# Performance work log

Hardware: AMD Instinct MI355X
Metric: run time of the kernel (lower is better)

The kernel has to match this reference:

```python
import jax, jax.numpy as jnp
import numpy as np

K = 10        # n_functions (random MLP draws)
H = 20        # hidden width of each tiny per-feature MLP
LN_EPS = 1e-5 # torch LayerNorm default eps
STD_EPS = 1e-8


def _layernorm(h):
    # LayerNorm over last dim, affine weight=1, bias=0 (torch default init),
    # biased variance, eps=1e-5.
    mu = h.mean(-1, keepdims=True)
    var = ((h - mu) ** 2).mean(-1, keepdims=True)
    return (h - mu) * jax.lax.rsqrt(var + LN_EPS)


def setup_inputs() -> dict:
    key = jax.random.key(0)
    B, T, N = 128, 256, 16
    ks = jax.random.split(key, 7)
    inputs = jax.random.normal(ks[0], (B, T, N), dtype=jnp.float32)

    def u(k, shape, bound):
        return jax.random.uniform(k, shape, minval=-bound, maxval=bound, dtype=jnp.float32)

    # torch Linear default init: uniform(-1/sqrt(fan_in), 1/sqrt(fan_in)) for W and b
    W1 = u(ks[1], (K, N, H), 1.0)        # Linear(1,20): fan_in=1
    b1 = u(ks[2], (K, N, H), 1.0)
    bnd = 1.0 / np.sqrt(H)
    W2 = u(ks[3], (K, N, H, H), bnd)     # Linear(20,20), weight layout [out,in]
    b2 = u(ks[4], (K, N, H), bnd)
    W3 = u(ks[5], (K, N, H), bnd)        # Linear(20,1) weight squeezed to [H]
    b3 = u(ks[6], (K, N), bnd)
    return {"inputs": inputs, "W1": W1, "b1": b1, "W2": W2, "b2": b2, "W3": W3, "b3": b3}


def reference(inputs, W1, b1, W2, b2, W3, b3):
    x = inputs.astype(jnp.float32)
    # standardize over batch dim (torch .std is unbiased, ddof=1)
    x = (x - x.mean(0)) / x.std(0, ddof=1)

    # All K draws x all N per-feature MLPs as one batched computation.
    # h: [K, B, T, N, H]
    h = jax.nn.relu(x[None, ..., None] * W1[:, None, None] + b1[:, None, None])
    h = _layernorm(h)
    h = jax.nn.relu(jnp.einsum('kbtni,knoi->kbtno', h, W2) + b2[:, None, None])
    h = _layernorm(h)
    t = jnp.einsum('kbtni,kni->kbtn', h, W3) + b3[:, None, None]   # [K, B, T, N]

    # std_out: standardize over batch dim
    t = (t - t.mean(1, keepdims=True)) / (t.std(1, ddof=1, keepdims=True) + STD_EPS)

    m_marginals = t.mean(1)                   # [K, T, N]
    prod_marginals = jnp.prod(m_marginals, -1)  # [K, T]
    prod_joint = jnp.prod(t, -1).mean(1)        # [K, T]
    per_k_mse = jnp.mean((prod_marginals - prod_joint) ** 2, axis=-1)  # [K]
    return jnp.mean(per_k_mse)
```

## Files before the change

kernel.cpp:

```cpp
#include <hip/hip_runtime.h>
#include <math.h>

#define B_ 128
#define T_ 256
#define N_ 16
#define K_ 10
#define H_ 20
#define TN_ 4096
#define TQ_ 128

#define REP20(F) F(0) F(1) F(2) F(3) F(4) F(5) F(6) F(7) F(8) F(9) \
                 F(10) F(11) F(12) F(13) F(14) F(15) F(16) F(17) F(18) F(19)

__device__ __forceinline__ float wsum(float v)
{
#pragma unroll
    for (int off = 32; off; off >>= 1) v += __shfl_xor(v, off);
    return v;
}

__global__ __launch_bounds__(256, 3) void k_all(
    const float* __restrict__ x,
    const float* __restrict__ W1, const float* __restrict__ b1,
    const float* __restrict__ W2, const float* __restrict__ b2,
    const float* __restrict__ W3, const float* __restrict__ b3,
    float* __restrict__ out)
{
    __shared__ float xz[32 * 129];
    __shared__ float zl[32 * 128];
    __shared__ float pjp[4];

    const int tq  = blockIdx.x;
    const int k   = blockIdx.y;
    const int tid = threadIdx.x;
    const int wv  = tid >> 6;
    const int l   = tid & 63;

#pragma unroll
    for (int r = 0; r < 4; ++r) {
        const int g4 = r * 1024 + tid * 4;
        const int b  = g4 >> 5;
        const int d0 = g4 & 31;
        const float4 v = *reinterpret_cast<const float4*>(x + b * TN_ + tq * 32 + d0);
        xz[(d0 + 0) * 129 + b] = v.x;
        xz[(d0 + 1) * 129 + b] = v.y;
        xz[(d0 + 2) * 129 + b] = v.z;
        xz[(d0 + 3) * 129 + b] = v.w;
    }
    __syncthreads();

#pragma unroll
    for (int c = 0; c < 8; ++c) {
        const int col = wv * 8 + c;
        const float a0 = xz[col * 129 + l];
        const float a1 = xz[col * 129 + 64 + l];
        const float mu = wsum(a0 + a1) * (1.f / 128.f);
        const float d0 = a0 - mu, d1 = a1 - mu;
        const float r  = __builtin_amdgcn_rsqf(wsum(fmaf(d0, d0, d1 * d1)) * (1.f / 127.f));
        xz[col * 129 + l]      = d0 * r;
        xz[col * 129 + 64 + l] = d1 * r;
    }
    __syncthreads();

#pragma unroll 1
    for (int it = 0; it < 8; ++it) {
        const int col = wv * 8 + it;
        const int kn  = k * 16 + (col & 15);

        const float u0 = xz[col * 129 + l];
        const float u1 = xz[col * 129 + 64 + l];

        const float4* __restrict__ w1v = reinterpret_cast<const float4*>(W1 + kn * 20);
        const float4* __restrict__ b1v = reinterpret_cast<const float4*>(b1 + kn * 20);
        const float4* __restrict__ w2v = reinterpret_cast<const float4*>(W2 + kn * 400);
        const float4* __restrict__ b2v = reinterpret_cast<const float4*>(b2 + kn * 20);
        const float4* __restrict__ w3v = reinterpret_cast<const float4*>(W3 + kn * 20);
        const float  bb3 = b3[kn];

#define DECLH(i) float ha##i, hb##i;
        REP20(DECLH)
        float s1a = 0.f, s1b = 0.f;
#define L1C(c,i0,i1,i2,i3) { const float4 w = w1v[c]; const float4 bb = b1v[c]; \
        ha##i0 = fmaxf(fmaf(u0, w.x, bb.x), 0.f); hb##i0 = fmaxf(fmaf(u1, w.x, bb.x), 0.f); s1a += ha##i0; s1b += hb##i0; \
        ha##i1 = fmaxf(fmaf(u0, w.y, bb.y), 0.f); hb##i1 = fmaxf(fmaf(u1, w.y, bb.y), 0.f); s1a += ha##i1; s1b += hb##i1; \
        ha##i2 = fmaxf(fmaf(u0, w.z, bb.z), 0.f); hb##i2 = fmaxf(fmaf(u1, w.z, bb.z), 0.f); s1a += ha##i2; s1b += hb##i2; \
        ha##i3 = fmaxf(fmaf(u0, w.w, bb.w), 0.f); hb##i3 = fmaxf(fmaf(u1, w.w, bb.w), 0.f); s1a += ha##i3; s1b += hb##i3; }
        L1C(0,0,1,2,3) L1C(1,4,5,6,7) L1C(2,8,9,10,11) L1C(3,12,13,14,15) L1C(4,16,17,18,19)

        const float mu1a = s1a * 0.05f, mu1b = s1b * 0.05f;
        float v1a = 0.f, v1b = 0.f;
#define VAR1(i) { float d = ha##i - mu1a; v1a = fmaf(d, d, v1a); d = hb##i - mu1b; v1b = fmaf(d, d, v1b); }
        REP20(VAR1)
        const float r1a = __builtin_amdgcn_rsqf(v1a * 0.05f + 1e-5f);
        const float r1b = __builtin_amdgcn_rsqf(v1b * 0.05f + 1e-5f);
        const float m1a = mu1a * r1a, m1b = mu1b * r1b;
#define NRM1(i) ha##i = fmaf(ha##i, r1a, -m1a); hb##i = fmaf(hb##i, r1b, -m1b);
        REP20(NRM1)

#define DECLG(i) float ga##i, gb##i;
        REP20(DECLG)
        float s2a = 0.f, s2b = 0.f;
#define L2C(o,c,i0,i1,i2,i3) { const float4 w = w2v[(o) * 5 + (c)]; \
        acca = fmaf(ha##i0, w.x, acca); acca = fmaf(ha##i1, w.y, acca); \
        acca = fmaf(ha##i2, w.z, acca); acca = fmaf(ha##i3, w.w, acca); \
        accb = fmaf(hb##i0, w.x, accb); accb = fmaf(hb##i1, w.y, accb); \
        accb = fmaf(hb##i2, w.z, accb); accb = fmaf(hb##i3, w.w, accb); }
#define L2ROW(o,bo) { float acca = (bo), accb = (bo); \
        L2C(o,0,0,1,2,3) L2C(o,1,4,5,6,7) L2C(o,2,8,9,10,11) \
        L2C(o,3,12,13,14,15) L2C(o,4,16,17,18,19) \
        ga##o = fmaxf(acca, 0.f); s2a += ga##o; gb##o = fmaxf(accb, 0.f); s2b += gb##o; }
        {
            const float4 b2c0 = b2v[0], b2c1 = b2v[1], b2c2 = b2v[2], b2c3 = b2v[3], b2c4 = b2v[4];
            L2ROW(0,  b2c0.x) L2ROW(1,  b2c0.y) L2ROW(2,  b2c0.z) L2ROW(3,  b2c0.w)
            L2ROW(4,  b2c1.x) L2ROW(5,  b2c1.y) L2ROW(6,  b2c1.z) L2ROW(7,  b2c1.w)
            L2ROW(8,  b2c2.x) L2ROW(9,  b2c2.y) L2ROW(10, b2c2.z) L2ROW(11, b2c2.w)
            L2ROW(12, b2c3.x) L2ROW(13, b2c3.y) L2ROW(14, b2c3.z) L2ROW(15, b2c3.w)
            L2ROW(16, b2c4.x) L2ROW(17, b2c4.y) L2ROW(18, b2c4.z) L2ROW(19, b2c4.w)
        }

        const float mu2a = s2a * 0.05f, mu2b = s2b * 0.05f;
        float v2a = 0.f, v2b = 0.f;
#define VAR2(i) { float d = ga##i - mu2a; v2a = fmaf(d, d, v2a); d = gb##i - mu2b; v2b = fmaf(d, d, v2b); }
        REP20(VAR2)
        const float r2a = __builtin_amdgcn_rsqf(v2a * 0.05f + 1e-5f);
        const float r2b = __builtin_amdgcn_rsqf(v2b * 0.05f + 1e-5f);
        const float m2a = mu2a * r2a, m2b = mu2b * r2b;

        float t0 = bb3, t1 = bb3;
#define L3C(c,i0,i1,i2,i3) { const float4 w = w3v[c]; \
        t0 = fmaf(fmaf(ga##i0, r2a, -m2a), w.x, t0); t1 = fmaf(fmaf(gb##i0, r2b, -m2b), w.x, t1); \
        t0 = fmaf(fmaf(ga##i1, r2a, -m2a), w.y, t0); t1 = fmaf(fmaf(gb##i1, r2b, -m2b), w.y, t1); \
        t0 = fmaf(fmaf(ga##i2, r2a, -m2a), w.z, t0); t1 = fmaf(fmaf(gb##i2, r2b, -m2b), w.z, t1); \
        t0 = fmaf(fmaf(ga##i3, r2a, -m2a), w.w, t0); t1 = fmaf(fmaf(gb##i3, r2b, -m2b), w.w, t1); }
        L3C(0,0,1,2,3) L3C(1,4,5,6,7) L3C(2,8,9,10,11) L3C(3,12,13,14,15) L3C(4,16,17,18,19)

        const float smu = wsum(t0 + t1) * (1.f / 128.f);
        const float e0 = t0 - smu, e1 = t1 - smu;
        const float sd = sqrtf(wsum(fmaf(e0, e0, e1 * e1)) * (1.f / 127.f));
        const float rr = 1.f / (sd + 1e-8f);
        zl[col * 128 + l]      = e0 * rr;
        zl[col * 128 + 64 + l] = e1 * rr;
    }
    __syncthreads();

    {
        const int t_loc = wv >> 1;
        const int b     = (wv & 1) * 64 + l;
        float pj = zl[(t_loc * 16 + 0) * 128 + b];
#pragma unroll
        for (int n = 1; n < 16; ++n) pj *= zl[(t_loc * 16 + n) * 128 + b];
        const float ps = wsum(pj);
        if (l == 0) pjp[wv] = ps;
    }
    __syncthreads();
    if (tid < 2) {
        const float pjm = (pjp[tid * 2] + pjp[tid * 2 + 1]) * (1.f / 128.f);
        atomicAdd(out, pjm * pjm * (1.f / (K_ * T_)));
    }
}

extern "C" void kernel_launch(void* const* d_in, const int* in_sizes, int n_in,
                              void* d_out, int out_size, void* d_ws, size_t ws_size,
                              hipStream_t stream)
{
    const float* x  = (const float*)d_in[0];
    const float* W1 = (const float*)d_in[1];
    const float* b1 = (const float*)d_in[2];
    const float* W2 = (const float*)d_in[3];
    const float* b2 = (const float*)d_in[4];
    const float* W3 = (const float*)d_in[5];
    const float* b3 = (const float*)d_in[6];
    float* out = (float*)d_out;

    hipMemsetAsync(out, 0, sizeof(float), stream);

    dim3 grid(TQ_, K_);
    k_all<<<grid, 256, 0, stream>>>(x, W1, b1, W2, b2, W3, b3, out);
}
```

Measured before the change: 236.4 us.

## Split blocks by (k,n) feature with global z buffer and last-block ticket reduction

Reorganizes the grid so each block handles one (k,n) MLP over a 32-timestep slab, which keeps that MLP's weights uniform per block and lets them be scalar-loaded instead of varying per wavefront. Standardized outputs go to a global workspace buffer. A ticket counter picks the last of 16 feature blocks for each slab to compute the product-over-N reduction, and a done counter finalizes the output. The cost is global-memory round trips for z, strided scalar input gathers, atomic and fence synchronization, a grid of only 1280 blocks, and launch bounds lowered to a single block per SIMD.

```diff
diff --git a/kernel.cpp b/kernel.cpp
--- a/kernel.cpp
+++ b/kernel.cpp
@@ -7,7 +7,8 @@
 #define K_ 10
 #define H_ 20
 #define TN_ 4096
-#define TQ_ 128
+#define TSLAB_ 32
+#define NTC_ 8
 
 #define REP20(F) F(0) F(1) F(2) F(3) F(4) F(5) F(6) F(7) F(8) F(9) \
                  F(10) F(11) F(12) F(13) F(14) F(15) F(16) F(17) F(18) F(19)
@@ -19,73 +20,64 @@
     return v;
 }
 
-__global__ __launch_bounds__(256, 3) void k_all(
+__global__ __launch_bounds__(256, 1) void k_fused(
     const float* __restrict__ x,
     const float* __restrict__ W1, const float* __restrict__ b1,
     const float* __restrict__ W2, const float* __restrict__ b2,
     const float* __restrict__ W3, const float* __restrict__ b3,
-    float* __restrict__ out)
+    float* __restrict__ out,
+    unsigned int* __restrict__ tickets,
+    unsigned int* __restrict__ done,
+    float* __restrict__ acc,
+    float* __restrict__ zbuf)
 {
-    __shared__ float xz[32 * 129];
-    __shared__ float zl[32 * 128];
-    __shared__ float pjp[4];
+    __shared__ float xz[TSLAB_ * 129];
+    __shared__ float wred[4];
+    __shared__ int   flag;
 
-    const int tq  = blockIdx.x;
-    const int k   = blockIdx.y;
+    const int tc  = blockIdx.x;
+    const int kn  = blockIdx.y;
+    const int k   = kn >> 4;
+    const int n   = kn & 15;
     const int tid = threadIdx.x;
     const int wv  = tid >> 6;
     const int l   = tid & 63;
 
 #pragma unroll
-    for (int r = 0; r < 4; ++r) {
-        const int g4 = r * 1024 + tid * 4;
-        const int b  = g4 >> 5;
-        const int d0 = g4 & 31;
-        const float4 v = *reinterpret_cast<const float4*>(x + b * TN_ + tq * 32 + d0);
-        xz[(d0 + 0) * 129 + b] = v.x;
-        xz[(d0 + 1) * 129 + b] = v.y;
-        xz[(d0 + 2) * 129 + b] = v.z;
-        xz[(d0 + 3) * 129 + b] = v.w;
+    for (int it = 0; it < 16; ++it) {
+        const int e   = it * 256 + tid;
+        const int col = e >> 7;
+        const int b   = e & 127;
+        xz[col * 129 + b] = x[b * TN_ + (tc * TSLAB_ + col) * N_ + n];
     }
     __syncthreads();
 
-#pragma unroll
-    for (int c = 0; c < 8; ++c) {
-        const int col = wv * 8 + c;
-        const float a0 = xz[col * 129 + l];
-        const float a1 = xz[col * 129 + 64 + l];
-        const float mu = wsum(a0 + a1) * (1.f / 128.f);
-        const float d0 = a0 - mu, d1 = a1 - mu;
-        const float r  = __builtin_amdgcn_rsqf(wsum(fmaf(d0, d0, d1 * d1)) * (1.f / 127.f));
-        xz[col * 129 + l]      = d0 * r;
-        xz[col * 129 + 64 + l] = d1 * r;
-    }
-    __syncthreads();
+    const float* __restrict__ w1c = W1 + kn * H_;
+    const float* __restrict__ b1c = b1 + kn * H_;
+    const float* __restrict__ w2c = W2 + kn * H_ * H_;
+    const float* __restrict__ b2c = b2 + kn * H_;
+    const float* __restrict__ w3c = W3 + kn * H_;
+    const float  bb3 = b3[kn];
 
 #pragma unroll 1
     for (int it = 0; it < 8; ++it) {
         const int col = wv * 8 + it;
-        const int kn  = k * 16 + (col & 15);
+        const int tg  = tc * TSLAB_ + col;
 
-        const float u0 = xz[col * 129 + l];
-        const float u1 = xz[col * 129 + 64 + l];
-
-        const float4* __restrict__ w1v = reinterpret_cast<const float4*>(W1 + kn * 20);
-        const float4* __restrict__ b1v = reinterpret_cast<const float4*>(b1 + kn * 20);
-        const float4* __restrict__ w2v = reinterpret_cast<const float4*>(W2 + kn * 400);
-        const float4* __restrict__ b2v = reinterpret_cast<const float4*>(b2 + kn * 20);
-        const float4* __restrict__ w3v = reinterpret_cast<const float4*>(W3 + kn * 20);
-        const float  bb3 = b3[kn];
+        const float a0 = xz[col * 129 + l];
+        const float a1 = xz[col * 129 + 64 + l];
+        const float xmu = wsum(a0 + a1) * (1.f / 128.f);
+        const float xd0 = a0 - xmu, xd1 = a1 - xmu;
+        const float xr  = __builtin_amdgcn_rsqf(wsum(fmaf(xd0, xd0, xd1 * xd1)) * (1.f / 127.f));
+        const float u0 = xd0 * xr, u1 = xd1 * xr;
 
 #define DECLH(i) float ha##i, hb##i;
         REP20(DECLH)
         float s1a = 0.f, s1b = 0.f;
-#define L1C(c,i0,i1,i2,i3) { const float4 w = w1v[c]; const float4 bb = b1v[c]; \
-        ha##i0 = fmaxf(fmaf(u0, w.x, bb.x), 0.f); hb##i0 = fmaxf(fmaf(u1, w.x, bb.x), 0.f); s1a += ha##i0; s1b += hb##i0; \
-        ha##i1 = fmaxf(fmaf(u0, w.y, bb.y), 0.f); hb##i1 = fmaxf(fmaf(u1, w.y, bb.y), 0.f); s1a += ha##i1; s1b += hb##i1; \
-        ha##i2 = fmaxf(fmaf(u0, w.z, bb.z), 0.f); hb##i2 = fmaxf(fmaf(u1, w.z, bb.z), 0.f); s1a += ha##i2; s1b += hb##i2; \
-        ha##i3 = fmaxf(fmaf(u0, w.w, bb.w), 0.f); hb##i3 = fmaxf(fmaf(u1, w.w, bb.w), 0.f); s1a += ha##i3; s1b += hb##i3; }
-        L1C(0,0,1,2,3) L1C(1,4,5,6,7) L1C(2,8,9,10,11) L1C(3,12,13,14,15) L1C(4,16,17,18,19)
+#define L1(i) { const float w = w1c[i], bb = b1c[i]; \
+        ha##i = fmaxf(fmaf(u0, w, bb), 0.f); s1a += ha##i; \
+        hb##i = fmaxf(fmaf(u1, w, bb), 0.f); s1b += hb##i; }
+        REP20(L1)
 
         const float mu1a = s1a * 0.05f, mu1b = s1b * 0.05f;
         float v1a = 0.f, v1b = 0.f;
@@ -100,23 +92,16 @@
 #define DECLG(i) float ga##i, gb##i;
         REP20(DECLG)
         float s2a = 0.f, s2b = 0.f;
-#define L2C(o,c,i0,i1,i2,i3) { const float4 w = w2v[(o) * 5 + (c)]; \
-        acca = fmaf(ha##i0, w.x, acca); acca = fmaf(ha##i1, w.y, acca); \
-        acca = fmaf(ha##i2, w.z, acca); acca = fmaf(ha##i3, w.w, acca); \
-        accb = fmaf(hb##i0, w.x, accb); accb = fmaf(hb##i1, w.y, accb); \
-        accb = fmaf(hb##i2, w.z, accb); accb = fmaf(hb##i3, w.w, accb); }
-#define L2ROW(o,bo) { float acca = (bo), accb = (bo); \
-        L2C(o,0,0,1,2,3) L2C(o,1,4,5,6,7) L2C(o,2,8,9,10,11) \
-        L2C(o,3,12,13,14,15) L2C(o,4,16,17,18,19) \
-        ga##o = fmaxf(acca, 0.f); s2a += ga##o; gb##o = fmaxf(accb, 0.f); s2b += gb##o; }
-        {
-            const float4 b2c0 = b2v[0], b2c1 = b2v[1], b2c2 = b2v[2], b2c3 = b2v[3], b2c4 = b2v[4];
-            L2ROW(0,  b2c0.x) L2ROW(1,  b2c0.y) L2ROW(2,  b2c0.z) L2ROW(3,  b2c0.w)
-            L2ROW(4,  b2c1.x) L2ROW(5,  b2c1.y) L2ROW(6,  b2c1.z) L2ROW(7,  b2c1.w)
-            L2ROW(8,  b2c2.x) L2ROW(9,  b2c2.y) L2ROW(10, b2c2.z) L2ROW(11, b2c2.w)
-            L2ROW(12, b2c3.x) L2ROW(13, b2c3.y) L2ROW(14, b2c3.z) L2ROW(15, b2c3.w)
-            L2ROW(16, b2c4.x) L2ROW(17, b2c4.y) L2ROW(18, b2c4.z) L2ROW(19, b2c4.w)
-        }
+#define L2I(o,i) { const float w = w2c[(o) * 20 + (i)]; \
+        acca = fmaf(ha##i, w, acca); accb = fmaf(hb##i, w, accb); }
+#define L2ALL(o) L2I(o,0) L2I(o,1) L2I(o,2) L2I(o,3) L2I(o,4) \
+        L2I(o,5) L2I(o,6) L2I(o,7) L2I(o,8) L2I(o,9) \
+        L2I(o,10) L2I(o,11) L2I(o,12) L2I(o,13) L2I(o,14) \
+        L2I(o,15) L2I(o,16) L2I(o,17) L2I(o,18) L2I(o,19)
+#define L2ROW(o) { float acca = b2c[o], accb = acca; L2ALL(o) \
+        ga##o = fmaxf(acca, 0.f); s2a += ga##o; \
+        gb##o = fmaxf(accb, 0.f); s2b += gb##o; }
+        REP20(L2ROW)
 
         const float mu2a = s2a * 0.05f, mu2b = s2b * 0.05f;
         float v2a = 0.f, v2b = 0.f;
@@ -127,35 +112,58 @@
         const float m2a = mu2a * r2a, m2b = mu2b * r2b;
 
         float t0 = bb3, t1 = bb3;
-#define L3C(c,i0,i1,i2,i3) { const float4 w = w3v[c]; \
-        t0 = fmaf(fmaf(ga##i0, r2a, -m2a), w.x, t0); t1 = fmaf(fmaf(gb##i0, r2b, -m2b), w.x, t1); \
-        t0 = fmaf(fmaf(ga##i1, r2a, -m2a), w.y, t0); t1 = fmaf(fmaf(gb##i1, r2b, -m2b), w.y, t1); \
-        t0 = fmaf(fmaf(ga##i2, r2a, -m2a), w.z, t0); t1 = fmaf(fmaf(gb##i2, r2b, -m2b), w.z, t1); \
-        t0 = fmaf(fmaf(ga##i3, r2a, -m2a), w.w, t0); t1 = fmaf(fmaf(gb##i3, r2b, -m2b), w.w, t1); }
-        L3C(0,0,1,2,3) L3C(1,4,5,6,7) L3C(2,8,9,10,11) L3C(3,12,13,14,15) L3C(4,16,17,18,19)
+#define L3(i) { const float w = w3c[i]; \
+        t0 = fmaf(fmaf(ga##i, r2a, -m2a), w, t0); \
+        t1 = fmaf(fmaf(gb##i, r2b, -m2b), w, t1); }
+        REP20(L3)
 
         const float smu = wsum(t0 + t1) * (1.f / 128.f);
         const float e0 = t0 - smu, e1 = t1 - smu;
         const float sd = sqrtf(wsum(fmaf(e0, e0, e1 * e1)) * (1.f / 127.f));
         const float rr = 1.f / (sd + 1e-8f);
-        zl[col * 128 + l]      = e0 * rr;
-        zl[col * 128 + 64 + l] = e1 * rr;
+        float* zg = zbuf + (((size_t)k * T_ + tg) * N_ + n) * B_;
+        zg[l]      = e0 * rr;
+        zg[64 + l] = e1 * rr;
+    }
+
+    __syncthreads();
+    if (tid == 0) {
+        __threadfence();
+        const unsigned int old = atomicAdd(&tickets[k * NTC_ + tc], 1u);
+        flag = (old == 15u);
     }
     __syncthreads();
+    if (!flag) return;
 
-    {
-        const int t_loc = wv >> 1;
-        const int b     = (wv & 1) * 64 + l;
-        float pj = zl[(t_loc * 16 + 0) * 128 + b];
+    if (tid == 0) __threadfence();
+    __syncthreads();
+
+    float part = 0.f;
+#pragma unroll 1
+    for (int c = 0; c < 8; ++c) {
+        const int tg = tc * TSLAB_ + wv * 8 + c;
+        const float* __restrict__ zrow = zbuf + ((size_t)k * T_ + tg) * (N_ * B_);
+        float p0 = zrow[l], p1 = zrow[64 + l];
 #pragma unroll
-        for (int n = 1; n < 16; ++n) pj *= zl[(t_loc * 16 + n) * 128 + b];
-        const float ps = wsum(pj);
-        if (l == 0) pjp[wv] = ps;
+        for (int nn = 1; nn < N_; ++nn) {
+            p0 *= zrow[nn * B_ + l];
+            p1 *= zrow[nn * B_ + 64 + l];
+        }
+        const float pj = wsum(p0 + p1) * (1.f / 128.f);
+        part += pj * pj;
     }
+    if (l == 0) wred[wv] = part;
     __syncthreads();
-    if (tid < 2) {
-        const float pjm = (pjp[tid * 2] + pjp[tid * 2 + 1]) * (1.f / 128.f);
-        atomicAdd(out, pjm * pjm * (1.f / (K_ * T_)));
+
+    if (tid == 0) {
+        const float s = (wred[0] + wred[1] + wred[2] + wred[3]) * (1.f / (K_ * T_));
+        atomicAdd(acc, s);
+        __threadfence();
+        const unsigned int d = atomicAdd(done, 1u);
+        if (d == 79u) {
+            const float tot = atomicAdd(acc, 0.f);
+            out[0] = tot;
+        }
     }
 }
 
@@ -172,8 +180,15 @@
     const float* b3 = (const float*)d_in[6];
     float* out = (float*)d_out;
 
-    hipMemsetAsync(out, 0, sizeof(float), stream);
+    char* ws = (char*)d_ws;
+    unsigned int* tickets = (unsigned int*)ws;
+    unsigned int* done    = (unsigned int*)(ws + 384);
+    float*        acc     = (float*)(ws + 512);
+    float*        zbuf    = (float*)(ws + 4096);
 
-    dim3 grid(TQ_, K_);
-    k_all<<<grid, 256, 0, stream>>>(x, W1, b1, W2, b2, W3, b3, out);
+    hipMemsetAsync(ws, 0, 1024, stream);
+
+    dim3 grid(NTC_, K_ * N_);
+    k_fused<<<grid, 256, 0, stream>>>(x, W1, b1, W2, b2, W3, b3,
+                                      out, tickets, done, acc, zbuf);
 }
```

Result: slower. 524.4 us (+121.8%).
